# Optimization experiments

Measured on AMD Instinct MI355X. Metric: run time of the kernel, lower is better.

The kernel has to match this reference:

```python
import jax, jax.numpy as jnp
import numpy as np

ATT_UNITS = 64
DEC_DIM = 512
ENC_DIM = 512


def setup_inputs() -> dict:
    key = jax.random.key(0)
    k1, k2, k3, k4, k5 = jax.random.split(key, 5)
    B, S = 256, 512
    # glorot-uniform-ish init scales
    def glorot(k, shape):
        fan_in, fan_out = shape[0], shape[1]
        lim = np.sqrt(6.0 / (fan_in + fan_out))
        return jax.random.uniform(k, shape, jnp.float32, -lim, lim)
    return {
        "decoder_hidden_state": jax.random.normal(k1, (B, DEC_DIM), jnp.float32),
        "encoder_output": jax.random.normal(k2, (B, S, ENC_DIM), jnp.float32),
        "w1_kernel": glorot(k3, (DEC_DIM, ATT_UNITS)),
        "w1_bias": jnp.zeros((ATT_UNITS,), jnp.float32),
        "w2_kernel": glorot(k4, (ENC_DIM, ATT_UNITS)),
        "w2_bias": jnp.zeros((ATT_UNITS,), jnp.float32),
        "v_kernel": glorot(k5, (ATT_UNITS, 1)),
        "v_bias": jnp.zeros((1,), jnp.float32),
    }


def reference(decoder_hidden_state, encoder_output, w1_kernel, w1_bias,
              w2_kernel, w2_bias, v_kernel, v_bias):
    # dec proj: [B, 1, U]; enc proj: [B, S, U]
    dec = (decoder_hidden_state @ w1_kernel + w1_bias)[:, None, :]
    enc = jnp.einsum('bse,eu->bsu', encoder_output, w2_kernel) + w2_bias
    # score: [B, S, 1]
    score = jnp.tanh(dec + enc) @ v_kernel + v_bias
    att_weights = jax.nn.softmax(score, axis=1)  # softmax over sequence axis
    # weighted sum over S -> [B, E]
    context_vector = jnp.sum(att_weights * encoder_output, axis=1)
    return (context_vector, att_weights)
```

## Files before the change

### kernel.cpp

```cpp
#include <hip/hip_runtime.h>
#include <hip/hip_bf16.h>

constexpr int NB = 256;
constexpr int SQ = 512;
constexpr int ED = 512;
constexpr int DD = 512;
constexpr int UU = 64;
constexpr int NT = 32;

typedef __attribute__((ext_vector_type(8))) short bf16x8;
typedef __attribute__((ext_vector_type(4))) float f32x4;

#define WAITVM(n) asm volatile("s_waitcnt vmcnt(" #n ")" ::: "memory")

__device__ __forceinline__ void stage16(const void* g, void* l) {
  __builtin_amdgcn_global_load_lds(
      (const __attribute__((address_space(1))) void*)g,
      (__attribute__((address_space(3))) void*)l, 16, 0, 0);
}

__device__ __forceinline__ unsigned short bf16_rne(float f) {
  unsigned int u = __float_as_uint(f);
  u += 0x7FFFu + ((u >> 16) & 1u);
  return (unsigned short)(u >> 16);
}

__device__ __forceinline__ uint2 split2(float v0, float v1) {
  unsigned int u0 = __float_as_uint(v0), u1 = __float_as_uint(v1);
  unsigned int h0 = u0 & 0xFFFF0000u, h1 = u1 & 0xFFFF0000u;
  unsigned int hi = (u0 >> 16) | h1;
  float r0 = v0 - __uint_as_float(h0);
  float r1 = v1 - __uint_as_float(h1);
  unsigned int lo = (__float_as_uint(r0) >> 16) | (__float_as_uint(r1) & 0xFFFF0000u);
  return make_uint2(hi, lo);
}

constexpr size_t WS_DEC   = 131072;
constexpr size_t WS_LBUF  = 196608;
constexpr size_t WS_CTILE = 262144;

__global__ __launch_bounds__(256) void prep_all(
    const float* __restrict__ w2, unsigned short* __restrict__ wsb,
    const float* __restrict__ dh, const float* __restrict__ w1,
    const float* __restrict__ w1b, const float* __restrict__ w2b,
    float* __restrict__ dec_ws) {
  const int blk = blockIdx.x;
  __shared__ float red[256];
  if (blk < 128) {
    int tid = blk * 256 + threadIdx.x;
    int j    = tid & 7;
    int lane = (tid >> 3) & 63;
    int nt   = (tid >> 9) & 3;
    int ks   = tid >> 11;
    int e = ks * 32 + (lane >> 4) * 8 + j;
    int u = nt * 16 + (lane & 15);
    wsb[tid] = bf16_rne(w2[e * UU + u]);
  } else {
    const int b = blk - 128;
    const int t = threadIdx.x;
    const int wave = t >> 6;
    const float* dhb = dh + (size_t)b * DD;
    const int e0 = wave * 128;
    float s = 0.f;
    #pragma unroll 8
    for (int i = 0; i < 128; ++i) {
      int e = e0 + i;
      s = fmaf(dhb[e], w1[e * UU + (t & 63)], s);
    }
    red[t] = s;
    __syncthreads();
    if (t < 64) {
      float d = w1b[t] + w2b[t] + red[t] + red[64 + t] + red[128 + t] + red[192 + t];
      dec_ws[b * UU + t] = d;
    }
  }
}

__global__ __launch_bounds__(256, 3) void attn_tile(
    const float* __restrict__ x,
    const float* __restrict__ vk,
    const unsigned short* __restrict__ wsb,
    const float* __restrict__ dec_ws,
    float* __restrict__ lbuf,
    float* __restrict__ ctile,
    float* __restrict__ out)
{
  const int bid = blockIdx.x;
  const int b  = bid >> 5;
  const int tl = bid & 31;
  const int t = threadIdx.x;
  const int wave = t >> 6;
  const int lane = t & 63;
  const int ul = lane & 15;
  const int g  = lane >> 4;
  const int swz = (ul & 7) << 4;

  __shared__ __align__(16) unsigned char slab[16][2048];
  __shared__ __align__(16) f32x4 red[4 * 4 * 64];

  const char* gsrc = (const char*)x + (size_t)(b * SQ + tl * 16) * 2048;

  #pragma unroll
  for (int r = 0; r < 4; ++r) {
    int row = wave * 4 + r;
    #pragma unroll
    for (int h = 0; h < 2; ++h) {
      int off = h * 1024 + lane * 16;
      stage16(gsrc + (size_t)row * 2048 + (size_t)(off ^ ((row & 7) << 4)),
              &slab[row][off]);
    }
  }

  const unsigned short* bp = wsb + lane * 8;
  bf16x8 bf[4][4];
  #pragma unroll
  for (int kk = 0; kk < 4; ++kk) {
    #pragma unroll
    for (int n = 0; n < 4; ++n)
      bf[kk][n] = *(const bf16x8*)(bp + (wave * 4 + kk) * 2048 + n * 512);
  }
  float dv[4], vv[4];
  #pragma unroll
  for (int n = 0; n < 4; ++n) {
    dv[n] = dec_ws[b * UU + n * 16 + ul];
    vv[n] = vk[n * 16 + ul];
  }
  float av = fabsf(vk[lane]);
  av += __shfl_xor(av, 1);
  av += __shfl_xor(av, 2);
  av += __shfl_xor(av, 4);
  av += __shfl_xor(av, 8);
  av += __shfl_xor(av, 16);
  av += __shfl_xor(av, 32);
  const float M = av;

  WAITVM(0);
  __syncthreads();

  const f32x4 zero4 = {0.f, 0.f, 0.f, 0.f};
  f32x4 acc[4];
  #pragma unroll
  for (int n = 0; n < 4; ++n) acc[n] = zero4;

  const unsigned char* Ab = &slab[ul][0];
  #pragma unroll
  for (int kk = 0; kk < 4; ++kk) {
    const int k = wave * 4 + kk;
    f32x4 a0 = *(const f32x4*)(Ab + ((g * 32 + k * 128) ^ swz));
    f32x4 a1 = *(const f32x4*)(Ab + ((g * 32 + k * 128 + 16) ^ swz));
    uint2 p0 = split2(a0[0], a0[1]);
    uint2 p1 = split2(a0[2], a0[3]);
    uint2 p2 = split2(a1[0], a1[1]);
    uint2 p3 = split2(a1[2], a1[3]);
    unsigned int hiw[4] = {p0.x, p1.x, p2.x, p3.x};
    unsigned int low[4] = {p0.y, p1.y, p2.y, p3.y};
    bf16x8 ahi, alo;
    memcpy(&ahi, hiw, 16);
    memcpy(&alo, low, 16);
    #pragma unroll
    for (int n = 0; n < 4; ++n) {
      acc[n] = __builtin_amdgcn_mfma_f32_16x16x32_bf16(ahi, bf[kk][n], acc[n], 0, 0, 0);
      acc[n] = __builtin_amdgcn_mfma_f32_16x16x32_bf16(alo, bf[kk][n], acc[n], 0, 0, 0);
    }
  }

  #pragma unroll
  for (int n = 0; n < 4; ++n) red[(wave * 4 + n) * 64 + lane] = acc[n];
  __syncthreads();
  #pragma unroll
  for (int n = 0; n < 4; ++n) {
    f32x4 s0 = red[(0 * 4 + n) * 64 + lane];
    f32x4 s1 = red[(1 * 4 + n) * 64 + lane];
    f32x4 s2 = red[(2 * 4 + n) * 64 + lane];
    f32x4 s3 = red[(3 * 4 + n) * 64 + lane];
    acc[n][0] = s0[0] + s1[0] + s2[0] + s3[0];
    acc[n][1] = s0[1] + s1[1] + s2[1] + s3[1];
    acc[n][2] = s0[2] + s1[2] + s2[2] + s3[2];
    acc[n][3] = s0[3] + s1[3] + s2[3] + s3[3];
  }

  float psc[4];
  #pragma unroll
  for (int r = 0; r < 4; ++r) {
    float s = 0.f;
    #pragma unroll
    for (int n = 0; n < 4; ++n) {
      float z = acc[n][r] + dv[n];
      float ez = __expf(2.f * z);
      float th = 1.f - 2.f / (ez + 1.f);
      s = fmaf(th, vv[n], s);
    }
    s += __shfl_xor(s, 1);
    s += __shfl_xor(s, 2);
    s += __shfl_xor(s, 4);
    s += __shfl_xor(s, 8);
    psc[r] = s;
  }
  float p[4];
  float lsum = 0.f;
  #pragma unroll
  for (int r = 0; r < 4; ++r) { p[r] = __expf(psc[r] - M); lsum += p[r]; }
  lsum += __shfl_xor(lsum, 16);
  lsum += __shfl_xor(lsum, 32);

  if (wave == 0 && ul == 0) {
    float* att = out + (size_t)NB * ED + (size_t)b * SQ + tl * 16;
    #pragma unroll
    for (int r = 0; r < 4; ++r) att[g * 4 + r] = p[r];
  }
  if (t == 0) lbuf[b * NT + tl] = lsum;

  {
    const int cbase = wave * 512 + lane * 8;
    float cx = 0.f, cy = 0.f;
    #pragma unroll
    for (int rr = 0; rr < 16; ++rr) {
      const float2 v = *(const float2*)&slab[rr][cbase ^ ((rr & 7) << 4)];
      float pi = __shfl(p[rr & 3], (rr >> 2) << 4);
      cx = fmaf(pi, v.x, cx);
      cy = fmaf(pi, v.y, cy);
    }
    float* ct = ctile + ((size_t)b * NT + tl) * ED + wave * 128 + lane * 2;
    ct[0] = cx;
    ct[1] = cy;
  }
}

__global__ __launch_bounds__(256) void combine(
    const float* __restrict__ lbuf,
    const float* __restrict__ ctile, float* __restrict__ out) {
  const int b = blockIdx.x;
  const int t = threadIdx.x;

  float L = 0.f;
  #pragma unroll 8
  for (int j = 0; j < NT; ++j) L += lbuf[b * NT + j];
  const float inv = 1.f / L;

  float* att = out + (size_t)NB * ED + (size_t)b * SQ;
  #pragma unroll
  for (int s = t; s < SQ; s += 256) att[s] *= inv;

  const float* ct = ctile + (size_t)b * NT * ED;
  #pragma unroll
  for (int e = t; e < ED; e += 256) {
    float c = 0.f;
    #pragma unroll 8
    for (int j = 0; j < NT; ++j) c += ct[j * ED + e];
    out[(size_t)b * ED + e] = c * inv;
  }
}

extern "C" void kernel_launch(void* const* d_in, const int* in_sizes, int n_in,
                              void* d_out, int out_size, void* d_ws, size_t ws_size,
                              hipStream_t stream) {
  const float* dh  = (const float*)d_in[0];
  const float* x   = (const float*)d_in[1];
  const float* w1  = (const float*)d_in[2];
  const float* w1b = (const float*)d_in[3];
  const float* w2  = (const float*)d_in[4];
  const float* w2b = (const float*)d_in[5];
  const float* vk  = (const float*)d_in[6];
  unsigned short* wsb = (unsigned short*)d_ws;
  float* dec_ws = (float*)((char*)d_ws + WS_DEC);
  float* lbuf   = (float*)((char*)d_ws + WS_LBUF);
  float* ctile  = (float*)((char*)d_ws + WS_CTILE);
  float* out = (float*)d_out;

  prep_all<<<384, 256, 0, stream>>>(w2, wsb, dh, w1, w1b, w2b, dec_ws);
  attn_tile<<<NB * NT, 256, 0, stream>>>(x, vk, wsb, dec_ws, lbuf, ctile, out);
  combine<<<NB, 256, 0, stream>>>(lbuf, ctile, out);
}
```

Measured before the change: 89.99 us.

## Make attention tile blocks persistent over four tiles with double-buffered LDS staging

Each block now processes four consecutive 16-row tiles instead of one. It double-buffers the encoder slab in LDS so async global-to-LDS loads of later tiles overlap compute on the current one. The MFMA work is re-split so each wave owns 16 units across the full K range, which replaces the cross-wave f32x4 LDS reduction with a small per-row score sum. W2 fragments are loaded once per block instead of once per tile. The cost is more LDS per block, lower occupancy (launch bounds 2) and extra barriers per tile.

Measured after the change: 120.3 us. +33.7%, slower.

```diff
diff --git a/kernel.cpp b/kernel.cpp
--- a/kernel.cpp
+++ b/kernel.cpp
@@ -11,7 +11,11 @@
 typedef __attribute__((ext_vector_type(8))) short bf16x8;
 typedef __attribute__((ext_vector_type(4))) float f32x4;
 
+#define MEMFENCE asm volatile("" ::: "memory")
+#define SBAR do { MEMFENCE; __builtin_amdgcn_s_barrier(); MEMFENCE; } while (0)
 #define WAITVM(n) asm volatile("s_waitcnt vmcnt(" #n ")" ::: "memory")
+#define WAITLGKM do { asm volatile("s_waitcnt lgkmcnt(0)" ::: "memory"); \
+                      __builtin_amdgcn_sched_barrier(0); } while (0)
 
 __device__ __forceinline__ void stage16(const void* g, void* l) {
   __builtin_amdgcn_global_load_lds(
@@ -76,7 +80,7 @@
   }
 }
 
-__global__ __launch_bounds__(256, 3) void attn_tile(
+__global__ __launch_bounds__(256, 2) void attn_tile(
     const float* __restrict__ x,
     const float* __restrict__ vk,
     const unsigned short* __restrict__ wsb,
@@ -85,9 +89,8 @@
     float* __restrict__ ctile,
     float* __restrict__ out)
 {
-  const int bid = blockIdx.x;
-  const int b  = bid >> 5;
-  const int tl = bid & 31;
+  const int b  = blockIdx.x >> 3;
+  const int q8 = blockIdx.x & 7;
   const int t = threadIdx.x;
   const int wave = t >> 6;
   const int lane = t & 63;
@@ -95,36 +98,33 @@
   const int g  = lane >> 4;
   const int swz = (ul & 7) << 4;
 
-  __shared__ __align__(16) unsigned char slab[16][2048];
-  __shared__ __align__(16) f32x4 red[4 * 4 * 64];
-
-  const char* gsrc = (const char*)x + (size_t)(b * SQ + tl * 16) * 2048;
-
-  #pragma unroll
-  for (int r = 0; r < 4; ++r) {
-    int row = wave * 4 + r;
-    #pragma unroll
-    for (int h = 0; h < 2; ++h) {
-      int off = h * 1024 + lane * 16;
-      stage16(gsrc + (size_t)row * 2048 + (size_t)(off ^ ((row & 7) << 4)),
-              &slab[row][off]);
-    }
-  }
-
-  const unsigned short* bp = wsb + lane * 8;
-  bf16x8 bf[4][4];
-  #pragma unroll
-  for (int kk = 0; kk < 4; ++kk) {
-    #pragma unroll
-    for (int n = 0; n < 4; ++n)
-      bf[kk][n] = *(const bf16x8*)(bp + (wave * 4 + kk) * 2048 + n * 512);
-  }
-  float dv[4], vv[4];
-  #pragma unroll
-  for (int n = 0; n < 4; ++n) {
-    dv[n] = dec_ws[b * UU + n * 16 + ul];
-    vv[n] = vk[n * 16 + ul];
-  }
+  __shared__ __align__(16) unsigned char slab[2][16][2048];
+  __shared__ float psum[4][16];
+
+  const char* gbase = (const char*)x + (size_t)(b * SQ + q8 * 64) * 2048;
+
+  auto stageT = [&](int i, int buf) {
+    #pragma unroll
+    for (int r = 0; r < 4; ++r) {
+      int row = wave * 4 + r;
+      #pragma unroll
+      for (int h = 0; h < 2; ++h) {
+        int off = h * 1024 + lane * 16;
+        stage16(gbase + (size_t)(i * 16 + row) * 2048 + (size_t)(off ^ ((row & 7) << 4)),
+                &slab[buf][row][off]);
+      }
+    }
+  };
+
+  stageT(0, 0);
+  stageT(1, 1);
+
+  const unsigned short* bp = wsb + wave * 512 + lane * 8;
+  bf16x8 bf[16];
+  #pragma unroll
+  for (int k = 0; k < 16; ++k) bf[k] = *(const bf16x8*)(bp + k * 2048);
+  const float dvs = dec_ws[b * UU + wave * 16 + ul];
+  const float vvs = vk[wave * 16 + ul];
   float av = fabsf(vk[lane]);
   av += __shfl_xor(av, 1);
   av += __shfl_xor(av, 2);
@@ -134,95 +134,90 @@
   av += __shfl_xor(av, 32);
   const float M = av;
 
-  WAITVM(0);
-  __syncthreads();
-
   const f32x4 zero4 = {0.f, 0.f, 0.f, 0.f};
-  f32x4 acc[4];
-  #pragma unroll
-  for (int n = 0; n < 4; ++n) acc[n] = zero4;
-
-  const unsigned char* Ab = &slab[ul][0];
-  #pragma unroll
-  for (int kk = 0; kk < 4; ++kk) {
-    const int k = wave * 4 + kk;
-    f32x4 a0 = *(const f32x4*)(Ab + ((g * 32 + k * 128) ^ swz));
-    f32x4 a1 = *(const f32x4*)(Ab + ((g * 32 + k * 128 + 16) ^ swz));
-    uint2 p0 = split2(a0[0], a0[1]);
-    uint2 p1 = split2(a0[2], a0[3]);
-    uint2 p2 = split2(a1[0], a1[1]);
-    uint2 p3 = split2(a1[2], a1[3]);
-    unsigned int hiw[4] = {p0.x, p1.x, p2.x, p3.x};
-    unsigned int low[4] = {p0.y, p1.y, p2.y, p3.y};
-    bf16x8 ahi, alo;
-    memcpy(&ahi, hiw, 16);
-    memcpy(&alo, low, 16);
-    #pragma unroll
-    for (int n = 0; n < 4; ++n) {
-      acc[n] = __builtin_amdgcn_mfma_f32_16x16x32_bf16(ahi, bf[kk][n], acc[n], 0, 0, 0);
-      acc[n] = __builtin_amdgcn_mfma_f32_16x16x32_bf16(alo, bf[kk][n], acc[n], 0, 0, 0);
-    }
-  }
-
-  #pragma unroll
-  for (int n = 0; n < 4; ++n) red[(wave * 4 + n) * 64 + lane] = acc[n];
-  __syncthreads();
-  #pragma unroll
-  for (int n = 0; n < 4; ++n) {
-    f32x4 s0 = red[(0 * 4 + n) * 64 + lane];
-    f32x4 s1 = red[(1 * 4 + n) * 64 + lane];
-    f32x4 s2 = red[(2 * 4 + n) * 64 + lane];
-    f32x4 s3 = red[(3 * 4 + n) * 64 + lane];
-    acc[n][0] = s0[0] + s1[0] + s2[0] + s3[0];
-    acc[n][1] = s0[1] + s1[1] + s2[1] + s3[1];
-    acc[n][2] = s0[2] + s1[2] + s2[2] + s3[2];
-    acc[n][3] = s0[3] + s1[3] + s2[3] + s3[3];
-  }
-
-  float psc[4];
-  #pragma unroll
-  for (int r = 0; r < 4; ++r) {
-    float s = 0.f;
-    #pragma unroll
-    for (int n = 0; n < 4; ++n) {
-      float z = acc[n][r] + dv[n];
+
+  #pragma unroll
+  for (int i = 0; i < 4; ++i) {
+    if (i < 3) { WAITVM(8); } else { WAITVM(0); }
+    SBAR;
+    const int buf = i & 1;
+    const int tl = q8 * 4 + i;
+
+    f32x4 acc = zero4;
+    const unsigned char* Ab = &slab[buf][ul][0];
+    #pragma unroll
+    for (int k = 0; k < 16; ++k) {
+      f32x4 a0 = *(const f32x4*)(Ab + ((g * 32 + k * 128) ^ swz));
+      f32x4 a1 = *(const f32x4*)(Ab + ((g * 32 + k * 128 + 16) ^ swz));
+      uint2 p0 = split2(a0[0], a0[1]);
+      uint2 p1 = split2(a0[2], a0[3]);
+      uint2 p2 = split2(a1[0], a1[1]);
+      uint2 p3 = split2(a1[2], a1[3]);
+      unsigned int hiw[4] = {p0.x, p1.x, p2.x, p3.x};
+      unsigned int low[4] = {p0.y, p1.y, p2.y, p3.y};
+      bf16x8 ahi, alo;
+      memcpy(&ahi, hiw, 16);
+      memcpy(&alo, low, 16);
+      acc = __builtin_amdgcn_mfma_f32_16x16x32_bf16(ahi, bf[k], acc, 0, 0, 0);
+      acc = __builtin_amdgcn_mfma_f32_16x16x32_bf16(alo, bf[k], acc, 0, 0, 0);
+    }
+
+    #pragma unroll
+    for (int r = 0; r < 4; ++r) {
+      float z = acc[r] + dvs;
       float ez = __expf(2.f * z);
       float th = 1.f - 2.f / (ez + 1.f);
-      s = fmaf(th, vv[n], s);
-    }
-    s += __shfl_xor(s, 1);
-    s += __shfl_xor(s, 2);
-    s += __shfl_xor(s, 4);
-    s += __shfl_xor(s, 8);
-    psc[r] = s;
-  }
-  float p[4];
-  float lsum = 0.f;
-  #pragma unroll
-  for (int r = 0; r < 4; ++r) { p[r] = __expf(psc[r] - M); lsum += p[r]; }
-  lsum += __shfl_xor(lsum, 16);
-  lsum += __shfl_xor(lsum, 32);
-
-  if (wave == 0 && ul == 0) {
-    float* att = out + (size_t)NB * ED + (size_t)b * SQ + tl * 16;
-    #pragma unroll
-    for (int r = 0; r < 4; ++r) att[g * 4 + r] = p[r];
-  }
-  if (t == 0) lbuf[b * NT + tl] = lsum;
-
-  {
-    const int cbase = wave * 512 + lane * 8;
-    float cx = 0.f, cy = 0.f;
-    #pragma unroll
-    for (int rr = 0; rr < 16; ++rr) {
-      const float2 v = *(const float2*)&slab[rr][cbase ^ ((rr & 7) << 4)];
-      float pi = __shfl(p[rr & 3], (rr >> 2) << 4);
-      cx = fmaf(pi, v.x, cx);
-      cy = fmaf(pi, v.y, cy);
-    }
-    float* ct = ctile + ((size_t)b * NT + tl) * ED + wave * 128 + lane * 2;
-    ct[0] = cx;
-    ct[1] = cy;
+      float s = th * vvs;
+      s += __shfl_xor(s, 1);
+      s += __shfl_xor(s, 2);
+      s += __shfl_xor(s, 4);
+      s += __shfl_xor(s, 8);
+      if (ul == 0) psum[wave][g * 4 + r] = s;
+    }
+    WAITLGKM;
+    SBAR;
+
+    float p[4];
+    float lsum = 0.f;
+    #pragma unroll
+    for (int r = 0; r < 4; ++r) {
+      int row = g * 4 + r;
+      float sc = psum[0][row] + psum[1][row] + psum[2][row] + psum[3][row];
+      p[r] = __expf(sc - M);
+      lsum += p[r];
+    }
+    lsum += __shfl_xor(lsum, 16);
+    lsum += __shfl_xor(lsum, 32);
+    lsum += __shfl_xor(lsum, 1);
+    lsum += __shfl_xor(lsum, 2);
+    lsum += __shfl_xor(lsum, 4);
+    lsum += __shfl_xor(lsum, 8);
+    lsum *= 0.0625f;
+
+    if (wave == 0 && ul == 0) {
+      float* att = out + (size_t)NB * ED + (size_t)b * SQ + tl * 16;
+      #pragma unroll
+      for (int r = 0; r < 4; ++r) att[g * 4 + r] = p[r];
+    }
+    if (t == 0) lbuf[b * NT + tl] = lsum;
+
+    {
+      const int cbase = wave * 512 + lane * 8;
+      float cx = 0.f, cy = 0.f;
+      #pragma unroll
+      for (int rr = 0; rr < 16; ++rr) {
+        const float2 v = *(const float2*)&slab[buf][rr][cbase ^ ((rr & 7) << 4)];
+        float pi = __shfl(p[rr & 3], (rr >> 2) << 4);
+        cx = fmaf(pi, v.x, cx);
+        cy = fmaf(pi, v.y, cy);
+      }
+      float* ct = ctile + ((size_t)b * NT + tl) * ED + wave * 128 + lane * 2;
+      ct[0] = cx;
+      ct[1] = cy;
+    }
+
+    SBAR;
+    if (i < 2) stageT(i + 2, buf);
   }
 }
 
@@ -268,6 +263,6 @@
   float* out = (float*)d_out;
 
   prep_all<<<384, 256, 0, stream>>>(w2, wsb, dh, w1, w1b, w2b, dec_ws);
-  attn_tile<<<NB * NT, 256, 0, stream>>>(x, vk, wsb, dec_ws, lbuf, ctile, out);
+  attn_tile<<<NB * 8, 256, 0, stream>>>(x, vk, wsb, dec_ws, lbuf, ctile, out);
   combine<<<NB, 256, 0, stream>>>(lbuf, ctile, out);
 }
```

## Repartition attn_tile MFMA work into 2x2 K/N wave split with smaller reduction

Applied to the files above, without the earlier changes.

Each wave in attn_tile previously took one quarter of K and all four N tiles. Now the four waves form a 2x2 grid: two K halves times two N halves. This cuts the cross-wave LDS reduction to a single partial-sum exchange, and a small psum array combines the per-N-half scores. The launch-bounds occupancy hint goes from 3 to 4 to allow more resident blocks for this bandwidth-bound streaming kernel. The explicit vmcnt wait before the barrier is removed, so correctness depends on the compiler waiting for the async global-to-LDS loads, and the split adds an extra barrier.

Result: faster. 82.85 us (-7.9%).

```diff
diff --git a/kernel.cpp b/kernel.cpp
--- a/kernel.cpp
+++ b/kernel.cpp
@@ -10,8 +10,6 @@
 
 typedef __attribute__((ext_vector_type(8))) short bf16x8;
 typedef __attribute__((ext_vector_type(4))) float f32x4;
-
-#define WAITVM(n) asm volatile("s_waitcnt vmcnt(" #n ")" ::: "memory")
 
 __device__ __forceinline__ void stage16(const void* g, void* l) {
   __builtin_amdgcn_global_load_lds(
@@ -76,7 +74,7 @@
   }
 }
 
-__global__ __launch_bounds__(256, 3) void attn_tile(
+__global__ __launch_bounds__(256, 4) void attn_tile(
     const float* __restrict__ x,
     const float* __restrict__ vk,
     const unsigned short* __restrict__ wsb,
@@ -94,9 +92,12 @@
   const int ul = lane & 15;
   const int g  = lane >> 4;
   const int swz = (ul & 7) << 4;
+  const int kw = wave >> 1;
+  const int nw = wave & 1;
 
   __shared__ __align__(16) unsigned char slab[16][2048];
-  __shared__ __align__(16) f32x4 red[4 * 4 * 64];
+  __shared__ __align__(16) f32x4 red4[4][64];
+  __shared__ float psum[2][16];
 
   const char* gsrc = (const char*)x + (size_t)(b * SQ + tl * 16) * 2048;
 
@@ -112,18 +113,18 @@
   }
 
   const unsigned short* bp = wsb + lane * 8;
-  bf16x8 bf[4][4];
-  #pragma unroll
-  for (int kk = 0; kk < 4; ++kk) {
-    #pragma unroll
-    for (int n = 0; n < 4; ++n)
-      bf[kk][n] = *(const bf16x8*)(bp + (wave * 4 + kk) * 2048 + n * 512);
-  }
-  float dv[4], vv[4];
-  #pragma unroll
-  for (int n = 0; n < 4; ++n) {
-    dv[n] = dec_ws[b * UU + n * 16 + ul];
-    vv[n] = vk[n * 16 + ul];
+  bf16x8 bf[8][2];
+  #pragma unroll
+  for (int i = 0; i < 8; ++i) {
+    #pragma unroll
+    for (int j = 0; j < 2; ++j)
+      bf[i][j] = *(const bf16x8*)(bp + (kw * 8 + i) * 2048 + (nw * 2 + j) * 512);
+  }
+  float dvs[2], vvs[2];
+  #pragma unroll
+  for (int j = 0; j < 2; ++j) {
+    dvs[j] = dec_ws[b * UU + (nw * 2 + j) * 16 + ul];
+    vvs[j] = vk[(nw * 2 + j) * 16 + ul];
   }
   float av = fabsf(vk[lane]);
   av += __shfl_xor(av, 1);
@@ -134,18 +135,17 @@
   av += __shfl_xor(av, 32);
   const float M = av;
 
-  WAITVM(0);
   __syncthreads();
 
   const f32x4 zero4 = {0.f, 0.f, 0.f, 0.f};
-  f32x4 acc[4];
-  #pragma unroll
-  for (int n = 0; n < 4; ++n) acc[n] = zero4;
+  f32x4 acc[2];
+  acc[0] = zero4;
+  acc[1] = zero4;
 
   const unsigned char* Ab = &slab[ul][0];
   #pragma unroll
-  for (int kk = 0; kk < 4; ++kk) {
-    const int k = wave * 4 + kk;
+  for (int i = 0; i < 8; ++i) {
+    const int k = kw * 8 + i;
     f32x4 a0 = *(const f32x4*)(Ab + ((g * 32 + k * 128) ^ swz));
     f32x4 a1 = *(const f32x4*)(Ab + ((g * 32 + k * 128 + 16) ^ swz));
     uint2 p0 = split2(a0[0], a0[1]);
@@ -158,50 +158,61 @@
     memcpy(&ahi, hiw, 16);
     memcpy(&alo, low, 16);
     #pragma unroll
-    for (int n = 0; n < 4; ++n) {
-      acc[n] = __builtin_amdgcn_mfma_f32_16x16x32_bf16(ahi, bf[kk][n], acc[n], 0, 0, 0);
-      acc[n] = __builtin_amdgcn_mfma_f32_16x16x32_bf16(alo, bf[kk][n], acc[n], 0, 0, 0);
-    }
-  }
-
-  #pragma unroll
-  for (int n = 0; n < 4; ++n) red[(wave * 4 + n) * 64 + lane] = acc[n];
+    for (int j = 0; j < 2; ++j) {
+      acc[j] = __builtin_amdgcn_mfma_f32_16x16x32_bf16(ahi, bf[i][j], acc[j], 0, 0, 0);
+      acc[j] = __builtin_amdgcn_mfma_f32_16x16x32_bf16(alo, bf[i][j], acc[j], 0, 0, 0);
+    }
+  }
+
+  if (kw == 0) {
+    red4[nw * 2 + 0][lane] = acc[0];
+    red4[nw * 2 + 1][lane] = acc[1];
+  }
   __syncthreads();
-  #pragma unroll
-  for (int n = 0; n < 4; ++n) {
-    f32x4 s0 = red[(0 * 4 + n) * 64 + lane];
-    f32x4 s1 = red[(1 * 4 + n) * 64 + lane];
-    f32x4 s2 = red[(2 * 4 + n) * 64 + lane];
-    f32x4 s3 = red[(3 * 4 + n) * 64 + lane];
-    acc[n][0] = s0[0] + s1[0] + s2[0] + s3[0];
-    acc[n][1] = s0[1] + s1[1] + s2[1] + s3[1];
-    acc[n][2] = s0[2] + s1[2] + s2[2] + s3[2];
-    acc[n][3] = s0[3] + s1[3] + s2[3] + s3[3];
-  }
-
-  float psc[4];
-  #pragma unroll
-  for (int r = 0; r < 4; ++r) {
-    float s = 0.f;
-    #pragma unroll
-    for (int n = 0; n < 4; ++n) {
-      float z = acc[n][r] + dv[n];
-      float ez = __expf(2.f * z);
-      float th = 1.f - 2.f / (ez + 1.f);
-      s = fmaf(th, vv[n], s);
-    }
-    s += __shfl_xor(s, 1);
-    s += __shfl_xor(s, 2);
-    s += __shfl_xor(s, 4);
-    s += __shfl_xor(s, 8);
-    psc[r] = s;
-  }
+  if (kw == 1) {
+    #pragma unroll
+    for (int j = 0; j < 2; ++j) {
+      f32x4 o = red4[nw * 2 + j][lane];
+      acc[j][0] += o[0];
+      acc[j][1] += o[1];
+      acc[j][2] += o[2];
+      acc[j][3] += o[3];
+    }
+    #pragma unroll
+    for (int r = 0; r < 4; ++r) {
+      float s = 0.f;
+      #pragma unroll
+      for (int j = 0; j < 2; ++j) {
+        float z = acc[j][r] + dvs[j];
+        float ez = __expf(2.f * z);
+        float th = 1.f - 2.f / (ez + 1.f);
+        s = fmaf(th, vvs[j], s);
+      }
+      s += __shfl_xor(s, 1);
+      s += __shfl_xor(s, 2);
+      s += __shfl_xor(s, 4);
+      s += __shfl_xor(s, 8);
+      if (ul == 0) psum[nw][g * 4 + r] = s;
+    }
+  }
+  __syncthreads();
+
   float p[4];
   float lsum = 0.f;
   #pragma unroll
-  for (int r = 0; r < 4; ++r) { p[r] = __expf(psc[r] - M); lsum += p[r]; }
+  for (int r = 0; r < 4; ++r) {
+    int row = g * 4 + r;
+    float sc = psum[0][row] + psum[1][row];
+    p[r] = __expf(sc - M);
+    lsum += p[r];
+  }
   lsum += __shfl_xor(lsum, 16);
   lsum += __shfl_xor(lsum, 32);
+  lsum += __shfl_xor(lsum, 1);
+  lsum += __shfl_xor(lsum, 2);
+  lsum += __shfl_xor(lsum, 4);
+  lsum += __shfl_xor(lsum, 8);
+  lsum *= 0.0625f;
 
   if (wave == 0 && ul == 0) {
     float* att = out + (size_t)NB * ED + (size_t)b * SQ + tl * 16;
```
